# Optimization experiments

Hardware: AMD Instinct MI355X
Metric: run time of the kernel (lower is better)

## Reference

```python
import jax, jax.numpy as jnp
import numpy as np

BN_EPS = 1e-3  # Keras BatchNormalization default epsilon

def setup_inputs() -> dict:
    key = jax.random.key(0)
    ks = jax.random.split(key, 6)
    B, H, W, C = 8, 128, 128, 128
    s = 0.05  # small init scale for weights
    return {
        "x1": jax.random.normal(ks[0], (B, H, W, C), jnp.float32),
        "x2": jax.random.normal(ks[1], (B, H, W, C), jnp.float32),
        "Wq": jax.random.normal(ks[2], (C, C), jnp.float32) * s,
        "Wk": jax.random.normal(ks[3], (C, C), jnp.float32) * s,
        "Wv": jax.random.normal(ks[4], (C, C), jnp.float32) * s,
        "Ws": jax.random.normal(ks[5], (C, C), jnp.float32) * s,
        "bs": jnp.zeros((C,), jnp.float32),
        "scale": jnp.ones((1,), jnp.float32),   # layers.Attention use_scale=True, init 1
        "gamma": jnp.ones((C,), jnp.float32),
        "beta": jnp.zeros((C,), jnp.float32),
        "mu": jnp.zeros((C,), jnp.float32),
        "var": jnp.ones((C,), jnp.float32),
    }


def reference(x1, x2, Wq, Wk, Wv, Ws, bs, scale, gamma, beta, mu, var):
    # x1, x2: [B,H,W,C].  1x1 convs with relu == per-pixel channel matmul.
    q = jax.nn.relu(jnp.einsum('bhwc,cd->bhwd', x1, Wq))  # [B,H,W,C]
    k = jax.nn.relu(jnp.einsum('bhwc,cd->bhwd', x1, Wk))
    v = jax.nn.relu(jnp.einsum('bhwc,cd->bhwd', x2, Wv))
    # After transpose [0,3,1,2], Keras Attention batches over (B,C):
    # seq axis = H (rows), feature dim = W (cols). Fold the transposes into einsum.
    scores = scale[0] * jnp.einsum('bhwc,bgwc->bchg', q, k)  # [B,C,H,H]
    attn = jax.nn.softmax(scores, axis=-1)
    # attn @ v over row axis g, then implicit transpose back to NHWC.
    o = jnp.einsum('bchg,bgwc->bhwc', attn, v)  # [B,H,W,C]
    # sigmoid 1x1 conv (with bias), then inference-mode BatchNorm.
    g = jax.nn.sigmoid(jnp.einsum('bhwc,cd->bhwd', o, Ws) + bs)
    g = gamma * (g - mu) * jax.lax.rsqrt(var + BN_EPS) + beta
    # gated residual
    return x1 + x2 * g
```

## Files before the change

### kernel.cpp

```cpp
#include <hip/hip_runtime.h>

typedef unsigned int u32;
typedef unsigned short u16;
typedef u16 u16x4 __attribute__((ext_vector_type(4)));
typedef u16 u16x8 __attribute__((ext_vector_type(8)));
typedef __bf16 bf16x8 __attribute__((ext_vector_type(8)));
typedef float f32x4 __attribute__((ext_vector_type(4)));

#define LDK 136
#define MFMA(a, b, c) __builtin_amdgcn_mfma_f32_16x16x32_bf16(a, b, c, 0, 0, 0)

__device__ __forceinline__ u16 f2b(float f) {
  u32 u = __builtin_bit_cast(u32, f);
  u = (u + 0x7fffu + ((u >> 16) & 1u)) >> 16;
  return (u16)u;
}
__device__ __forceinline__ float b2f(u16 h) {
  u32 u = ((u32)h) << 16;
  return __builtin_bit_cast(float, u);
}

__global__ void wprep(const float* __restrict__ Wq, const float* __restrict__ Wk,
                      const float* __restrict__ Wv, const float* __restrict__ Ws,
                      u16* __restrict__ wT) {
  const float* srcs[4] = {Wq, Wk, Wv, Ws};
  const float* s = srcs[blockIdx.x];
  u16* d = wT + (size_t)blockIdx.x * 16384;
  for (int idx = threadIdx.x; idx < 16384; idx += 256) {
    int i = idx >> 7, j = idx & 127;
    d[j * 128 + i] = f2b(s[idx]);
  }
}

__global__ __launch_bounds__(256, 1)
void qkv_kernel(const float* __restrict__ x1, const float* __restrict__ x2,
                const u16* __restrict__ wT,
                u16* __restrict__ q_t, u16* __restrict__ k_t, u16* __restrict__ v_t) {
  __shared__ u16 Xs[128 * LDK];
  __shared__ u16 WT[128 * LDK];
  __shared__ u16 ST[128 * LDK];

  const int t = threadIdx.x;
  const int bh = blockIdx.x;
  const int b = bh >> 7, h = bh & 127;
  const size_t pixbase = (size_t)bh * 16384;
  const size_t obase = (size_t)b * 2097152 + (size_t)h * 128;

#pragma unroll
  for (int j = 0; j < 8; ++j) {
    int lin = j * 256 + t;
    int w = lin >> 4, c0 = (lin & 15) << 3;
    f32x4 a0 = *(const f32x4*)&x1[pixbase + lin * 8];
    f32x4 a1 = *(const f32x4*)&x1[pixbase + lin * 8 + 4];
    u16x8 p;
#pragma unroll
    for (int i = 0; i < 4; ++i) { p[i] = f2b(a0[i]); p[4 + i] = f2b(a1[i]); }
    *(u16x8*)&Xs[w * LDK + c0] = p;
  }

  const int lane = t & 63, wave = t >> 6;
  const int lrow = lane & 15, lq = lane >> 4;
  const int nstrip = wave * 32;

  u16* outs[3] = {q_t, k_t, v_t};

  for (int m = 0; m < 3; ++m) {
    if (m == 2) {
#pragma unroll
      for (int j = 0; j < 8; ++j) {
        int lin = j * 256 + t;
        int w = lin >> 4, c0 = (lin & 15) << 3;
        f32x4 a0 = *(const f32x4*)&x2[pixbase + lin * 8];
        f32x4 a1 = *(const f32x4*)&x2[pixbase + lin * 8 + 4];
        u16x8 p;
#pragma unroll
        for (int i = 0; i < 4; ++i) { p[i] = f2b(a0[i]); p[4 + i] = f2b(a1[i]); }
        *(u16x8*)&Xs[w * LDK + c0] = p;
      }
    }
#pragma unroll
    for (int j = 0; j < 8; ++j) {
      int lin = j * 256 + t;
      int r = lin >> 4, c0 = (lin & 15) << 3;
      *(u16x8*)&WT[r * LDK + c0] = *(const u16x8*)&wT[(size_t)m * 16384 + lin * 8];
    }
    __syncthreads();

    f32x4 acc[8][2];
#pragma unroll
    for (int mt = 0; mt < 8; ++mt) {
      acc[mt][0] = (f32x4){0.f, 0.f, 0.f, 0.f};
      acc[mt][1] = (f32x4){0.f, 0.f, 0.f, 0.f};
    }
#pragma unroll
    for (int kk = 0; kk < 4; ++kk) {
      int ko = kk * 32 + lq * 8;
      bf16x8 b0 = *(const bf16x8*)&WT[(nstrip + lrow) * LDK + ko];
      bf16x8 b1 = *(const bf16x8*)&WT[(nstrip + 16 + lrow) * LDK + ko];
#pragma unroll
      for (int mt = 0; mt < 8; ++mt) {
        bf16x8 a = *(const bf16x8*)&Xs[(mt * 16 + lrow) * LDK + ko];
        acc[mt][0] = MFMA(a, b0, acc[mt][0]);
        acc[mt][1] = MFMA(a, b1, acc[mt][1]);
      }
    }
    __syncthreads();

#pragma unroll
    for (int mt = 0; mt < 8; ++mt) {
      int w0 = mt * 16 + lq * 4;
#pragma unroll
      for (int nt = 0; nt < 2; ++nt) {
        int c = nstrip + nt * 16 + lrow;
        u16x4 p;
#pragma unroll
        for (int r = 0; r < 4; ++r) p[r] = f2b(fmaxf(acc[mt][nt][r], 0.f));
        *(u16x4*)&ST[c * LDK + w0] = p;
      }
    }
    __syncthreads();

    u16* dst = outs[m];
    {
      int c = t >> 1, w0 = (t & 1) * 64;
#pragma unroll
      for (int j = 0; j < 8; ++j)
        *(u16x8*)&dst[obase + (size_t)c * 16384 + w0 + j * 8] =
            *(const u16x8*)&ST[c * LDK + w0 + j * 8];
    }
    __syncthreads();
  }
}

__global__ __launch_bounds__(256, 1)
void attn_kernel(u16* __restrict__ q_t, const u16* __restrict__ k_t,
                 const u16* __restrict__ v_t, const float* __restrict__ scale_p) {
  __shared__ u16 Ks[128 * LDK];
  __shared__ u16 QP[128 * LDK];
  __shared__ u16 Vt[128 * LDK];

  const int t = threadIdx.x;
  const size_t base = (size_t)blockIdx.x * 16384;

#pragma unroll
  for (int j = 0; j < 8; ++j) {
    int lin = j * 256 + t;
    int r = lin >> 4, c0 = (lin & 15) << 3;
    *(u16x8*)&QP[r * LDK + c0] = *(const u16x8*)&q_t[base + lin * 8];
    *(u16x8*)&Ks[r * LDK + c0] = *(const u16x8*)&k_t[base + lin * 8];
  }
  {
    int g0 = (t & 15) * 8, w0 = (t >> 4) * 8;
    u16 vv[8][8];
#pragma unroll
    for (int i = 0; i < 8; ++i)
      *(u16x8*)&vv[i][0] = *(const u16x8*)&v_t[base + (g0 + i) * 128 + w0];
#pragma unroll
    for (int j = 0; j < 8; ++j) {
      u16x8 tv;
#pragma unroll
      for (int i = 0; i < 8; ++i) tv[i] = vv[i][j];
      *(u16x8*)&Vt[(w0 + j) * LDK + g0] = tv;
    }
  }
  __syncthreads();

  const int lane = t & 63, wave = t >> 6;
  const int lrow = lane & 15, lq = lane >> 4;
  const int hstrip = wave * 32;
  const float scl = scale_p[0];

  f32x4 acc[8][2];
#pragma unroll
  for (int mt = 0; mt < 8; ++mt) {
    acc[mt][0] = (f32x4){0.f, 0.f, 0.f, 0.f};
    acc[mt][1] = (f32x4){0.f, 0.f, 0.f, 0.f};
  }
#pragma unroll
  for (int kk = 0; kk < 4; ++kk) {
    int ko = kk * 32 + lq * 8;
    bf16x8 b0 = *(const bf16x8*)&QP[(hstrip + lrow) * LDK + ko];
    bf16x8 b1 = *(const bf16x8*)&QP[(hstrip + 16 + lrow) * LDK + ko];
#pragma unroll
    for (int mt = 0; mt < 8; ++mt) {
      bf16x8 a = *(const bf16x8*)&Ks[(mt * 16 + lrow) * LDK + ko];
      acc[mt][0] = MFMA(a, b0, acc[mt][0]);
      acc[mt][1] = MFMA(a, b1, acc[mt][1]);
    }
  }

  float inv[2];
#pragma unroll
  for (int nt = 0; nt < 2; ++nt) {
    float mx = -1e30f;
#pragma unroll
    for (int mt = 0; mt < 8; ++mt)
#pragma unroll
      for (int r = 0; r < 4; ++r) {
        acc[mt][nt][r] *= scl;
        mx = fmaxf(mx, acc[mt][nt][r]);
      }
    mx = fmaxf(mx, __shfl_xor(mx, 16));
    mx = fmaxf(mx, __shfl_xor(mx, 32));
    float s = 0.f;
#pragma unroll
    for (int mt = 0; mt < 8; ++mt)
#pragma unroll
      for (int r = 0; r < 4; ++r) {
        float e = __expf(acc[mt][nt][r] - mx);
        acc[mt][nt][r] = e;
        s += e;
      }
    s += __shfl_xor(s, 16);
    s += __shfl_xor(s, 32);
    inv[nt] = 1.f / s;
  }
  __syncthreads();

#pragma unroll
  for (int mt = 0; mt < 8; ++mt) {
    int g0 = mt * 16 + lq * 4;
#pragma unroll
    for (int nt = 0; nt < 2; ++nt) {
      int hh = hstrip + nt * 16 + lrow;
      u16x4 p;
#pragma unroll
      for (int r = 0; r < 4; ++r) p[r] = f2b(acc[mt][nt][r] * inv[nt]);
      *(u16x4*)&QP[hh * LDK + g0] = p;
    }
  }
  __syncthreads();

  f32x4 o[8][2];
#pragma unroll
  for (int mt = 0; mt < 8; ++mt) {
    o[mt][0] = (f32x4){0.f, 0.f, 0.f, 0.f};
    o[mt][1] = (f32x4){0.f, 0.f, 0.f, 0.f};
  }
#pragma unroll
  for (int kk = 0; kk < 4; ++kk) {
    int ko = kk * 32 + lq * 8;
    bf16x8 b0 = *(const bf16x8*)&QP[(hstrip + lrow) * LDK + ko];
    bf16x8 b1 = *(const bf16x8*)&QP[(hstrip + 16 + lrow) * LDK + ko];
#pragma unroll
    for (int mt = 0; mt < 8; ++mt) {
      bf16x8 a = *(const bf16x8*)&Vt[(mt * 16 + lrow) * LDK + ko];
      o[mt][0] = MFMA(a, b0, o[mt][0]);
      o[mt][1] = MFMA(a, b1, o[mt][1]);
    }
  }

#pragma unroll
  for (int mt = 0; mt < 8; ++mt) {
    int w0 = mt * 16 + lq * 4;
#pragma unroll
    for (int nt = 0; nt < 2; ++nt) {
      int hh = hstrip + nt * 16 + lrow;
      u16x4 p;
#pragma unroll
      for (int r = 0; r < 4; ++r) p[r] = f2b(o[mt][nt][r]);
      *(u16x4*)&Ks[hh * LDK + w0] = p;
    }
  }
  __syncthreads();

  {
    int hh = t >> 1, w0 = (t & 1) * 64;
#pragma unroll
    for (int j = 0; j < 8; ++j)
      *(u16x8*)&q_t[base + hh * 128 + w0 + j * 8] =
          *(const u16x8*)&Ks[hh * LDK + w0 + j * 8];
  }
}

__global__ __launch_bounds__(256, 2)
void final_kernel(const u16* __restrict__ o_t, const u16* __restrict__ wsT,
                  const float* __restrict__ x1, const float* __restrict__ x2,
                  const float* __restrict__ bs, const float* __restrict__ gamma,
                  const float* __restrict__ beta, const float* __restrict__ mu,
                  const float* __restrict__ var, float* __restrict__ out) {
  __shared__ u16 Os[128 * LDK];
  __shared__ u16 WT[128 * LDK];
  __shared__ float bnA[128], bnB[128], bsf[128];

  const int t = threadIdx.x;
  const int bh = blockIdx.x;
  const int b = bh >> 7, h = bh & 127;
  const size_t obase = (size_t)b * 2097152 + (size_t)h * 128;
  const size_t pixbase = (size_t)bh * 16384;

  if (t < 128) {
    float a = gamma[t] * rsqrtf(var[t] + 1e-3f);
    bnA[t] = a;
    bnB[t] = beta[t] - mu[t] * a;
    bsf[t] = bs[t];
  }
#pragma unroll
  for (int j = 0; j < 8; ++j) {
    int lin = j * 256 + t;
    int r = lin >> 4, c0 = (lin & 15) << 3;
    *(u16x8*)&WT[r * LDK + c0] = *(const u16x8*)&wsT[lin * 8];
  }
  {
    int c0 = (t & 15) * 8, w0 = (t >> 4) * 8;
    u16 ov[8][8];
#pragma unroll
    for (int i = 0; i < 8; ++i)
      *(u16x8*)&ov[i][0] = *(const u16x8*)&o_t[obase + (size_t)(c0 + i) * 16384 + w0];
#pragma unroll
    for (int j = 0; j < 8; ++j) {
      u16x8 tv;
#pragma unroll
      for (int i = 0; i < 8; ++i) tv[i] = ov[i][j];
      *(u16x8*)&Os[(w0 + j) * LDK + c0] = tv;
    }
  }
  __syncthreads();

  const int lane = t & 63, wave = t >> 6;
  const int lrow = lane & 15, lq = lane >> 4;
  const int wstrip = wave * 32;

  f32x4 acc[8][2];
#pragma unroll
  for (int mt = 0; mt < 8; ++mt) {
    acc[mt][0] = (f32x4){0.f, 0.f, 0.f, 0.f};
    acc[mt][1] = (f32x4){0.f, 0.f, 0.f, 0.f};
  }
#pragma unroll
  for (int kk = 0; kk < 4; ++kk) {
    int ko = kk * 32 + lq * 8;
    bf16x8 b0 = *(const bf16x8*)&Os[(wstrip + lrow) * LDK + ko];
    bf16x8 b1 = *(const bf16x8*)&Os[(wstrip + 16 + lrow) * LDK + ko];
#pragma unroll
    for (int mt = 0; mt < 8; ++mt) {
      bf16x8 a = *(const bf16x8*)&WT[(mt * 16 + lrow) * LDK + ko];
      acc[mt][0] = MFMA(a, b0, acc[mt][0]);
      acc[mt][1] = MFMA(a, b1, acc[mt][1]);
    }
  }
  __syncthreads();

#pragma unroll
  for (int mt = 0; mt < 8; ++mt) {
    int d0 = mt * 16 + lq * 4;
#pragma unroll
    for (int nt = 0; nt < 2; ++nt) {
      int w = wstrip + nt * 16 + lrow;
      u16x4 p;
#pragma unroll
      for (int r = 0; r < 4; ++r) {
        int d = d0 + r;
        float sv = acc[mt][nt][r] + bsf[d];
        float sg = 1.f / (1.f + __expf(-sv));
        p[r] = f2b(bnA[d] * sg + bnB[d]);
      }
      *(u16x4*)&Os[w * LDK + d0] = p;
    }
  }
  __syncthreads();

  {
    int w = t >> 1, d0 = (t & 1) * 64;
#pragma unroll
    for (int j = 0; j < 8; ++j) {
      int d = d0 + j * 8;
      u16x8 g8 = *(const u16x8*)&Os[w * LDK + d];
      f32x4 a0 = *(const f32x4*)&x1[pixbase + w * 128 + d];
      f32x4 a1 = *(const f32x4*)&x1[pixbase + w * 128 + d + 4];
      f32x4 c0v = *(const f32x4*)&x2[pixbase + w * 128 + d];
      f32x4 c1v = *(const f32x4*)&x2[pixbase + w * 128 + d + 4];
      f32x4 r0, r1;
#pragma unroll
      for (int i = 0; i < 4; ++i) {
        r0[i] = a0[i] + c0v[i] * b2f(g8[i]);
        r1[i] = a1[i] + c1v[i] * b2f(g8[4 + i]);
      }
      *(f32x4*)&out[pixbase + w * 128 + d] = r0;
      *(f32x4*)&out[pixbase + w * 128 + d + 4] = r1;
    }
  }
}

extern "C" void kernel_launch(void* const* d_in, const int* in_sizes, int n_in,
                              void* d_out, int out_size, void* d_ws, size_t ws_size,
                              hipStream_t stream) {
  const float* x1 = (const float*)d_in[0];
  const float* x2 = (const float*)d_in[1];
  const float* Wq = (const float*)d_in[2];
  const float* Wk = (const float*)d_in[3];
  const float* Wv = (const float*)d_in[4];
  const float* Ws = (const float*)d_in[5];
  const float* bs = (const float*)d_in[6];
  const float* scale = (const float*)d_in[7];
  const float* gamma = (const float*)d_in[8];
  const float* beta = (const float*)d_in[9];
  const float* mu = (const float*)d_in[10];
  const float* var = (const float*)d_in[11];
  float* outp = (float*)d_out;

  u16* q_t = (u16*)d_ws;
  u16* k_t = q_t + 16777216;
  u16* v_t = k_t + 16777216;
  u16* wT = v_t + 16777216;

  wprep<<<dim3(4), dim3(256), 0, stream>>>(Wq, Wk, Wv, Ws, wT);
  qkv_kernel<<<dim3(1024), dim3(256), 0, stream>>>(x1, x2, wT, q_t, k_t, v_t);
  attn_kernel<<<dim3(1024), dim3(256), 0, stream>>>(q_t, k_t, v_t, scale);
  final_kernel<<<dim3(1024), dim3(256), 0, stream>>>(q_t, wT + 3 * 16384, x1, x2, bs,
                                                     gamma, beta, mu, var, outp);
}
```

Baseline: 355.8 us.

## Cut LDS footprint by reading weights from global and reusing buffers

The qkv and final kernels now read the bf16 weight fragments straight from global memory (L2/L1 cached) into registers instead of staging them in LDS. The attention kernel drops its separate V buffer: V is prefetched into registers during softmax and transposed into the K buffer after QK^T is done. These LDS savings let launch bounds rise to 2 or 3 blocks per CU to increase occupancy and latency hiding, at the cost of more global/cache traffic for weights in the final kernel's inner loop and extra register pressure.

```diff
diff --git a/kernel.cpp b/kernel.cpp
--- a/kernel.cpp
+++ b/kernel.cpp
@@ -32,12 +32,11 @@
   }
 }
 
-__global__ __launch_bounds__(256, 1)
+__global__ __launch_bounds__(256, 2)
 void qkv_kernel(const float* __restrict__ x1, const float* __restrict__ x2,
                 const u16* __restrict__ wT,
                 u16* __restrict__ q_t, u16* __restrict__ k_t, u16* __restrict__ v_t) {
   __shared__ u16 Xs[128 * LDK];
-  __shared__ u16 WT[128 * LDK];
   __shared__ u16 ST[128 * LDK];
 
   const int t = threadIdx.x;
@@ -57,6 +56,7 @@
     for (int i = 0; i < 4; ++i) { p[i] = f2b(a0[i]); p[4 + i] = f2b(a1[i]); }
     *(u16x8*)&Xs[w * LDK + c0] = p;
   }
+  __syncthreads();
 
   const int lane = t & 63, wave = t >> 6;
   const int lrow = lane & 15, lq = lane >> 4;
@@ -65,6 +65,15 @@
   u16* outs[3] = {q_t, k_t, v_t};
 
   for (int m = 0; m < 3; ++m) {
+    const u16* wb = wT + (size_t)m * 16384;
+    bf16x8 w0[4], w1[4];
+#pragma unroll
+    for (int kk = 0; kk < 4; ++kk) {
+      int ko = kk * 32 + lq * 8;
+      w0[kk] = *(const bf16x8*)&wb[(nstrip + lrow) * 128 + ko];
+      w1[kk] = *(const bf16x8*)&wb[(nstrip + 16 + lrow) * 128 + ko];
+    }
+
     if (m == 2) {
 #pragma unroll
       for (int j = 0; j < 8; ++j) {
@@ -77,14 +86,8 @@
         for (int i = 0; i < 4; ++i) { p[i] = f2b(a0[i]); p[4 + i] = f2b(a1[i]); }
         *(u16x8*)&Xs[w * LDK + c0] = p;
       }
-    }
-#pragma unroll
-    for (int j = 0; j < 8; ++j) {
-      int lin = j * 256 + t;
-      int r = lin >> 4, c0 = (lin & 15) << 3;
-      *(u16x8*)&WT[r * LDK + c0] = *(const u16x8*)&wT[(size_t)m * 16384 + lin * 8];
-    }
-    __syncthreads();
+      __syncthreads();
+    }
 
     f32x4 acc[8][2];
 #pragma unroll
@@ -95,49 +98,45 @@
 #pragma unroll
     for (int kk = 0; kk < 4; ++kk) {
       int ko = kk * 32 + lq * 8;
-      bf16x8 b0 = *(const bf16x8*)&WT[(nstrip + lrow) * LDK + ko];
-      bf16x8 b1 = *(const bf16x8*)&WT[(nstrip + 16 + lrow) * LDK + ko];
 #pragma unroll
       for (int mt = 0; mt < 8; ++mt) {
         bf16x8 a = *(const bf16x8*)&Xs[(mt * 16 + lrow) * LDK + ko];
-        acc[mt][0] = MFMA(a, b0, acc[mt][0]);
-        acc[mt][1] = MFMA(a, b1, acc[mt][1]);
+        acc[mt][0] = MFMA(a, w0[kk], acc[mt][0]);
+        acc[mt][1] = MFMA(a, w1[kk], acc[mt][1]);
       }
     }
     __syncthreads();
 
 #pragma unroll
     for (int mt = 0; mt < 8; ++mt) {
-      int w0 = mt * 16 + lq * 4;
+      int w0i = mt * 16 + lq * 4;
 #pragma unroll
       for (int nt = 0; nt < 2; ++nt) {
         int c = nstrip + nt * 16 + lrow;
         u16x4 p;
 #pragma unroll
         for (int r = 0; r < 4; ++r) p[r] = f2b(fmaxf(acc[mt][nt][r], 0.f));
-        *(u16x4*)&ST[c * LDK + w0] = p;
+        *(u16x4*)&ST[c * LDK + w0i] = p;
       }
     }
     __syncthreads();
 
     u16* dst = outs[m];
     {
-      int c = t >> 1, w0 = (t & 1) * 64;
+      int c = t >> 1, w0i = (t & 1) * 64;
 #pragma unroll
       for (int j = 0; j < 8; ++j)
-        *(u16x8*)&dst[obase + (size_t)c * 16384 + w0 + j * 8] =
-            *(const u16x8*)&ST[c * LDK + w0 + j * 8];
-    }
-    __syncthreads();
-  }
-}
-
-__global__ __launch_bounds__(256, 1)
+        *(u16x8*)&dst[obase + (size_t)c * 16384 + w0i + j * 8] =
+            *(const u16x8*)&ST[c * LDK + w0i + j * 8];
+    }
+  }
+}
+
+__global__ __launch_bounds__(256, 2)
 void attn_kernel(u16* __restrict__ q_t, const u16* __restrict__ k_t,
                  const u16* __restrict__ v_t, const float* __restrict__ scale_p) {
   __shared__ u16 Ks[128 * LDK];
   __shared__ u16 QP[128 * LDK];
-  __shared__ u16 Vt[128 * LDK];
 
   const int t = threadIdx.x;
   const size_t base = (size_t)blockIdx.x * 16384;
@@ -149,20 +148,6 @@
     *(u16x8*)&QP[r * LDK + c0] = *(const u16x8*)&q_t[base + lin * 8];
     *(u16x8*)&Ks[r * LDK + c0] = *(const u16x8*)&k_t[base + lin * 8];
   }
-  {
-    int g0 = (t & 15) * 8, w0 = (t >> 4) * 8;
-    u16 vv[8][8];
-#pragma unroll
-    for (int i = 0; i < 8; ++i)
-      *(u16x8*)&vv[i][0] = *(const u16x8*)&v_t[base + (g0 + i) * 128 + w0];
-#pragma unroll
-    for (int j = 0; j < 8; ++j) {
-      u16x8 tv;
-#pragma unroll
-      for (int i = 0; i < 8; ++i) tv[i] = vv[i][j];
-      *(u16x8*)&Vt[(w0 + j) * LDK + g0] = tv;
-    }
-  }
   __syncthreads();
 
   const int lane = t & 63, wave = t >> 6;
@@ -189,6 +174,12 @@
     }
   }
 
+  const int g0 = (t & 15) * 8, w0v = (t >> 4) * 8;
+  u16x8 vv[8];
+#pragma unroll
+  for (int i = 0; i < 8; ++i)
+    vv[i] = *(const u16x8*)&v_t[base + (g0 + i) * 128 + w0v];
+
   float inv[2];
 #pragma unroll
   for (int nt = 0; nt < 2; ++nt) {
@@ -218,15 +209,22 @@
   __syncthreads();
 
 #pragma unroll
-  for (int mt = 0; mt < 8; ++mt) {
-    int g0 = mt * 16 + lq * 4;
+  for (int j = 0; j < 8; ++j) {
+    u16x8 tv;
+#pragma unroll
+    for (int i = 0; i < 8; ++i) tv[i] = vv[i][j];
+    *(u16x8*)&Ks[(w0v + j) * LDK + g0] = tv;
+  }
+#pragma unroll
+  for (int mt = 0; mt < 8; ++mt) {
+    int gg0 = mt * 16 + lq * 4;
 #pragma unroll
     for (int nt = 0; nt < 2; ++nt) {
       int hh = hstrip + nt * 16 + lrow;
       u16x4 p;
 #pragma unroll
       for (int r = 0; r < 4; ++r) p[r] = f2b(acc[mt][nt][r] * inv[nt]);
-      *(u16x4*)&QP[hh * LDK + g0] = p;
+      *(u16x4*)&QP[hh * LDK + gg0] = p;
     }
   }
   __syncthreads();
@@ -244,43 +242,43 @@
     bf16x8 b1 = *(const bf16x8*)&QP[(hstrip + 16 + lrow) * LDK + ko];
 #pragma unroll
     for (int mt = 0; mt < 8; ++mt) {
-      bf16x8 a = *(const bf16x8*)&Vt[(mt * 16 + lrow) * LDK + ko];
+      bf16x8 a = *(const bf16x8*)&Ks[(mt * 16 + lrow) * LDK + ko];
       o[mt][0] = MFMA(a, b0, o[mt][0]);
       o[mt][1] = MFMA(a, b1, o[mt][1]);
     }
   }
-
-#pragma unroll
-  for (int mt = 0; mt < 8; ++mt) {
-    int w0 = mt * 16 + lq * 4;
+  __syncthreads();
+
+#pragma unroll
+  for (int mt = 0; mt < 8; ++mt) {
+    int w0i = mt * 16 + lq * 4;
 #pragma unroll
     for (int nt = 0; nt < 2; ++nt) {
       int hh = hstrip + nt * 16 + lrow;
       u16x4 p;
 #pragma unroll
       for (int r = 0; r < 4; ++r) p[r] = f2b(o[mt][nt][r]);
-      *(u16x4*)&Ks[hh * LDK + w0] = p;
+      *(u16x4*)&Ks[hh * LDK + w0i] = p;
     }
   }
   __syncthreads();
 
   {
-    int hh = t >> 1, w0 = (t & 1) * 64;
+    int hh = t >> 1, w0i = (t & 1) * 64;
 #pragma unroll
     for (int j = 0; j < 8; ++j)
-      *(u16x8*)&q_t[base + hh * 128 + w0 + j * 8] =
-          *(const u16x8*)&Ks[hh * LDK + w0 + j * 8];
-  }
-}
-
-__global__ __launch_bounds__(256, 2)
+      *(u16x8*)&q_t[base + hh * 128 + w0i + j * 8] =
+          *(const u16x8*)&Ks[hh * LDK + w0i + j * 8];
+  }
+}
+
+__global__ __launch_bounds__(256, 3)
 void final_kernel(const u16* __restrict__ o_t, const u16* __restrict__ wsT,
                   const float* __restrict__ x1, const float* __restrict__ x2,
                   const float* __restrict__ bs, const float* __restrict__ gamma,
                   const float* __restrict__ beta, const float* __restrict__ mu,
                   const float* __restrict__ var, float* __restrict__ out) {
   __shared__ u16 Os[128 * LDK];
-  __shared__ u16 WT[128 * LDK];
   __shared__ float bnA[128], bnB[128], bsf[128];
 
   const int t = threadIdx.x;
@@ -295,12 +293,6 @@
     bnB[t] = beta[t] - mu[t] * a;
     bsf[t] = bs[t];
   }
-#pragma unroll
-  for (int j = 0; j < 8; ++j) {
-    int lin = j * 256 + t;
-    int r = lin >> 4, c0 = (lin & 15) << 3;
-    *(u16x8*)&WT[r * LDK + c0] = *(const u16x8*)&wsT[lin * 8];
-  }
   {
     int c0 = (t & 15) * 8, w0 = (t >> 4) * 8;
     u16 ov[8][8];
@@ -334,7 +326,7 @@
     bf16x8 b1 = *(const bf16x8*)&Os[(wstrip + 16 + lrow) * LDK + ko];
 #pragma unroll
     for (int mt = 0; mt < 8; ++mt) {
-      bf16x8 a = *(const bf16x8*)&WT[(mt * 16 + lrow) * LDK + ko];
+      bf16x8 a = *(const bf16x8*)&wsT[(mt * 16 + lrow) * 128 + ko];
       acc[mt][0] = MFMA(a, b0, acc[mt][0]);
       acc[mt][1] = MFMA(a, b1, acc[mt][1]);
     }
```

New measurement: 360.9 us. Within noise of the previous version (+1.4%).
